# Optimization experiments

Measured on AMD Instinct MI355X. Metric: run time of the kernel, lower is better.

## Reference

```python
import jax, jax.numpy as jnp
import numpy as np

N, E, F, H, G, C = 50000, 800000, 128, 64, 512, 10
RATIO = 0.5  # forward arg `ratio` baked as constant


def seg_mean(msgs, idx, n):
    s = jax.ops.segment_sum(msgs, idx, num_segments=n)
    cnt = jax.ops.segment_sum(jnp.ones(idx.shape[0], msgs.dtype), idx, num_segments=n)
    return s / jnp.maximum(cnt, 1.0)[:, None]


def sage(x, src, dst, Wl, bl, Wr, ew=None):
    # PyG SAGEConv: lin_l(mean_{j->i} msg_j) + lin_r(x_i); weighted variant scales messages
    m = x[src] if ew is None else x[src] * ew[:, None]
    agg = seg_mean(m, dst, x.shape[0])
    return agg @ Wl + bl + x @ Wr


def topk_mask(scores, seg, num_graphs, ratio):
    # per-graph (segment) top-k edge selection: keep ceil(ratio*edges_in_graph) highest scores
    e = scores.shape[0]
    counts = jax.ops.segment_sum(jnp.ones(e, jnp.float32), seg, num_segments=num_graphs)
    order = jnp.lexsort((-scores, seg))  # sort by segment, then score descending
    seg_sorted = seg[order]
    starts = jnp.concatenate([jnp.zeros(1, jnp.float32), jnp.cumsum(counts)[:-1]])
    rank = jnp.arange(e, dtype=jnp.float32) - starts[seg_sorted]
    k = jnp.ceil(ratio * counts)
    sel = (rank < k[seg_sorted]).astype(scores.dtype)
    return jnp.zeros(e, scores.dtype).at[order].set(sel)


def setup_inputs():
    key = jax.random.key(0)
    ks = jax.random.split(key, 16)
    w = lambda k, shape, fan: (jax.random.normal(k, shape, jnp.float32) / np.sqrt(fan))
    return {
        'x': jax.random.normal(ks[0], (N, F), jnp.float32),
        'edge_index': jax.random.randint(ks[1], (2, E), 0, N, jnp.int32),
        'batch': jnp.sort(jax.random.randint(ks[2], (N,), 0, G, jnp.int32)),
        'W1l': w(ks[3], (F, H), F), 'b1l': jnp.zeros(H, jnp.float32), 'W1r': w(ks[4], (F, H), F),
        'W2l': w(ks[5], (H, H), H), 'b2l': jnp.zeros(H, jnp.float32), 'W2r': w(ks[6], (H, H), H),
        'W3l': w(ks[7], (H, H), H), 'b3l': jnp.zeros(H, jnp.float32), 'W3r': w(ks[8], (H, H), H),
        'Wlin1': w(ks[9], (H, H), H), 'blin1': jnp.zeros(H, jnp.float32),
        'Wlin2': w(ks[10], (H, C), H), 'blin2': jnp.zeros(C, jnp.float32),
    }


def reference(x, edge_index, batch, W1l, b1l, W1r, W2l, b2l, W2r, W3l, b3l, W3r, Wlin1, blin1, Wlin2, blin2):
    src, dst = edge_index[0], edge_index[1]
    h = jax.nn.relu(sage(x, src, dst, W1l, b1l, W1r))
    edge_scores = jnp.sum(h[src] * h[dst], axis=-1)  # [E]
    seg = batch[src]  # graph id per edge (sections)
    sampled = topk_mask(edge_scores, seg, G, RATIO)
    ew = edge_scores * sampled
    h = jax.nn.relu(sage(h, src, dst, W2l, b2l, W2r, ew))
    h = jax.nn.relu(sage(h, src, dst, W3l, b3l, W3r, ew))
    pooled = seg_mean(h, batch, G)  # global_mean_pool
    z = jax.nn.relu(pooled @ Wlin1 + blin1)
    z = z @ Wlin2 + blin2  # dropout inactive in eval
    return jax.nn.log_softmax(z, axis=-1), sampled
```

## Files before the change

### kernel.cpp

```cpp
#include <hip/hip_runtime.h>
#include <hip/hip_bf16.h>
#include <math.h>

static constexpr int N = 50000;
static constexpr int E = 800000;
static constexpr int F = 128;
static constexpr int H = 64;
static constexpr int G = 512;
static constexpr int C = 10;
static constexpr int CAP = 256;
static constexpr int NFB = (E / 4 + 255) / 256;
static constexpr int GB1 = N / 16;
static constexpr int GB2 = (N + 31) / 32;
static constexpr int SB = E / 256;

static inline int cdiv(long a, int b) { return (int)((a + b - 1) / b); }

__device__ __forceinline__ float uinv_score(unsigned u) {
  return (u & 0x80000000u) ? __uint_as_float(u & 0x7fffffffu) : __uint_as_float(~u);
}

__device__ __forceinline__ int2 pack_slot(int s, int d, int g, int e) {
  unsigned a = (unsigned)s | ((unsigned)(d & 0x7FFF) << 17);
  unsigned b = ((unsigned)d >> 15) | ((unsigned)g << 2) | ((unsigned)e << 11);
  return make_int2((int)a, (int)b);
}
__device__ __forceinline__ int slot_src(int2 p) { return p.x & 0x1FFFF; }
__device__ __forceinline__ int slot_dst(int2 p) {
  return (int)(((unsigned)p.x >> 17) | (((unsigned)p.y & 3u) << 15));
}
__device__ __forceinline__ int slot_g(int2 p) { return (int)(((unsigned)p.y >> 2) & 0x1FFu); }
__device__ __forceinline__ int slot_eid(int2 p) { return (int)((unsigned)p.y >> 11); }

__global__ void k_deg_goff(const int* __restrict__ dst, const int* __restrict__ batch,
                           int* __restrict__ deg, int* __restrict__ goff,
                           unsigned short* __restrict__ rank16) {
  int tid = threadIdx.x;
  for (int i = blockIdx.x * 256 + tid; i < N; i += gridDim.x * 256) {
    int b = batch[i];
    if (i == 0) {
      for (int g = 0; g <= b; ++g) goff[g] = 0;
    } else {
      int p = batch[i - 1];
      for (int g = p + 1; g <= b; ++g) goff[g] = i;
    }
    if (i == N - 1) {
      for (int g = b + 1; g <= G; ++g) goff[g] = N;
    }
  }
  const int4* d4 = (const int4*)dst;
  for (int i = blockIdx.x * 256 + tid; i < E / 4; i += gridDim.x * 256) {
    int4 v = d4[i];
    ushort4 rk;
    rk.x = (unsigned short)atomicAdd(&deg[v.x], 1);
    rk.y = (unsigned short)atomicAdd(&deg[v.y], 1);
    rk.z = (unsigned short)atomicAdd(&deg[v.z], 1);
    rk.w = (unsigned short)atomicAdd(&deg[v.w], 1);
    *(ushort4*)(rank16 + (size_t)i * 4) = rk;
  }
}

__global__ void k_scan_a(const int* __restrict__ cnt, int* __restrict__ off,
                         int* __restrict__ bsum, int n) {
  __shared__ int wsum[16];
  int tid = threadIdx.x, lane = tid & 63, wv = tid >> 6;
  int idx = blockIdx.x * 4096 + tid * 4;
  int v0 = (idx + 0 < n) ? cnt[idx + 0] : 0;
  int v1 = (idx + 1 < n) ? cnt[idx + 1] : 0;
  int v2 = (idx + 2 < n) ? cnt[idx + 2] : 0;
  int v3 = (idx + 3 < n) ? cnt[idx + 3] : 0;
  int local = v0 + v1 + v2 + v3;
  int inc = local;
  for (int d = 1; d < 64; d <<= 1) {
    int t = __shfl_up(inc, d);
    if (lane >= d) inc += t;
  }
  if (lane == 63) wsum[wv] = inc;
  __syncthreads();
  if (tid < 16) {
    int t = wsum[tid];
    for (int d = 1; d < 16; d <<= 1) {
      int u = __shfl_up(t, d);
      if (tid >= d) t += u;
    }
    wsum[tid] = t;
  }
  __syncthreads();
  int woff = (wv > 0) ? wsum[wv - 1] : 0;
  int excl = woff + inc - local;
  if (idx + 0 < n) off[idx + 0] = excl;
  if (idx + 1 < n) off[idx + 1] = excl + v0;
  if (idx + 2 < n) off[idx + 2] = excl + v0 + v1;
  if (idx + 3 < n) off[idx + 3] = excl + v0 + v1 + v2;
  if (tid == 0) bsum[blockIdx.x] = wsum[15];
}

__global__ void k_scan_c(int* __restrict__ off, const int* __restrict__ bsum, int n, int nb) {
  __shared__ int spre[34];
  int tid = threadIdx.x;
  if (tid < 32) {
    int v = (tid < nb) ? bsum[tid] : 0;
    int inc = v;
    for (int d = 1; d < 32; d <<= 1) {
      int t = __shfl_up(inc, d);
      if (tid >= d) inc += t;
    }
    spre[tid] = inc - v;
  }
  __syncthreads();
  int i = blockIdx.x * 256 + tid;
  if (i < n) {
    off[i] = off[i] + spre[i >> 12];
  } else if (i == n) {
    off[n] = spre[nb];
  }
}

__global__ void k_fill_gemm(const int* __restrict__ src, const int* __restrict__ dst,
                            const unsigned short* __restrict__ rank16,
                            const int* __restrict__ batch, const int* __restrict__ off,
                            int2* __restrict__ csrp, int* __restrict__ einv,
                            const float* __restrict__ x, const float* __restrict__ Wl,
                            const float* __restrict__ Wr, const float* __restrict__ bl,
                            float* __restrict__ y, float* __restrict__ r) {
  __shared__ float sx[16][F];
  int lane = threadIdx.x, ty = threadIdx.y;
  int tid = ty * 64 + lane;
  int bq = blockIdx.x / 5, br = blockIdx.x - bq * 5;
  if (br == 0) {
    int i = bq * 256 + tid;
    if (i < E / 4) {
      int4 dv = ((const int4*)dst)[i];
      int4 sv = ((const int4*)src)[i];
      ushort4 rv = *(const ushort4*)(rank16 + (size_t)i * 4);
      int dd[4] = {dv.x, dv.y, dv.z, dv.w};
      int ss[4] = {sv.x, sv.y, sv.z, sv.w};
      int rr[4] = {rv.x, rv.y, rv.z, rv.w};
      int e0 = i * 4;
      int slots[4];
#pragma unroll
      for (int j = 0; j < 4; ++j) {
        int g = batch[ss[j]];
        int slot = off[dd[j]] + rr[j];
        csrp[slot] = pack_slot(ss[j], dd[j], g, e0 + j);
        slots[j] = slot;
      }
      *(int4*)(einv + e0) = make_int4(slots[0], slots[1], slots[2], slots[3]);
    }
    return;
  }
  int gid = bq * 4 + (br - 1);
  if (gid >= GB1) return;
  int row0 = gid * 16;
  const float4* gsrc = (const float4*)(x + (size_t)row0 * F);
  float4* sdst = (float4*)(&sx[0][0]);
#pragma unroll
  for (int i = tid; i < 16 * F / 4; i += 256) sdst[i] = gsrc[i];
  __syncthreads();
  float al[4], ar[4];
  float bias = bl[lane];
#pragma unroll
  for (int j = 0; j < 4; ++j) { al[j] = 0.f; ar[j] = bias; }
#pragma unroll 4
  for (int f = 0; f < F; ++f) {
    float wl = Wl[f * H + lane];
    float wr = Wr[f * H + lane];
#pragma unroll
    for (int j = 0; j < 4; ++j) {
      float xv = sx[ty * 4 + j][f];
      al[j] += xv * wl;
      ar[j] += xv * wr;
    }
  }
#pragma unroll
  for (int j = 0; j < 4; ++j) {
    int row = row0 + ty * 4 + j;
    y[(size_t)row * H + lane] = al[j];
    r[(size_t)row * H + lane] = ar[j];
  }
}

template <int K>
__global__ void k_gemm2h(const float* __restrict__ in, const float* __restrict__ Wl,
                         const float* __restrict__ Wr, const float* __restrict__ b,
                         __hip_bfloat16* __restrict__ y, float* __restrict__ r) {
  __shared__ float sx[16][K];
  int lane = threadIdx.x, ty = threadIdx.y;
  int tid = ty * 64 + lane;
  int row0 = blockIdx.x * 16;
  const float4* gsrc = (const float4*)(in + (size_t)row0 * K);
  float4* sdst = (float4*)(&sx[0][0]);
#pragma unroll
  for (int i = tid; i < 16 * K / 4; i += 256) sdst[i] = gsrc[i];
  __syncthreads();
  float al[4], ar[4];
  float bias = b[lane];
#pragma unroll
  for (int j = 0; j < 4; ++j) { al[j] = 0.f; ar[j] = bias; }
#pragma unroll 4
  for (int f = 0; f < K; ++f) {
    float wl = Wl[f * H + lane];
    float wr = Wr[f * H + lane];
#pragma unroll
    for (int j = 0; j < 4; ++j) {
      float xv = sx[ty * 4 + j][f];
      al[j] += xv * wl;
      ar[j] += xv * wr;
    }
  }
#pragma unroll
  for (int j = 0; j < 4; ++j) {
    int row = row0 + ty * 4 + j;
    y[(size_t)row * H + lane] = __float2bfloat16(al[j]);
    r[(size_t)row * H + lane] = ar[j];
  }
}

__global__ void k_agg1(const float* __restrict__ y, const float* __restrict__ r,
                       const int2* __restrict__ csrp, const int* __restrict__ off,
                       float* __restrict__ out) {
  int node = blockIdx.x * 8 + threadIdx.y;
  int lane = threadIdx.x;
  int q = lane >> 3, c = lane & 7;
  int s0 = off[node], s1 = off[node + 1];
  float4 a0 = make_float4(0.f, 0.f, 0.f, 0.f);
  float4 a1 = make_float4(0.f, 0.f, 0.f, 0.f);
  int i = s0 + q;
  for (; i + 8 < s1; i += 16) {
    int se0 = slot_src(csrp[i]);
    int se1 = slot_src(csrp[i + 8]);
    const float4* p0 = (const float4*)(y + (size_t)se0 * H);
    const float4* p1 = (const float4*)(y + (size_t)se1 * H);
    float4 u0 = p0[c], v0 = p0[c + 8];
    float4 u1 = p1[c], v1 = p1[c + 8];
    a0.x += u0.x + u1.x; a0.y += u0.y + u1.y; a0.z += u0.z + u1.z; a0.w += u0.w + u1.w;
    a1.x += v0.x + v1.x; a1.y += v0.y + v1.y; a1.z += v0.z + v1.z; a1.w += v0.w + v1.w;
  }
  for (; i < s1; i += 8) {
    int se = slot_src(csrp[i]);
    const float4* p = (const float4*)(y + (size_t)se * H);
    float4 u = p[c], v = p[c + 8];
    a0.x += u.x; a0.y += u.y; a0.z += u.z; a0.w += u.w;
    a1.x += v.x; a1.y += v.y; a1.z += v.z; a1.w += v.w;
  }
#pragma unroll
  for (int d = 8; d < 64; d <<= 1) {
    a0.x += __shfl_xor(a0.x, d); a0.y += __shfl_xor(a0.y, d);
    a0.z += __shfl_xor(a0.z, d); a0.w += __shfl_xor(a0.w, d);
    a1.x += __shfl_xor(a1.x, d); a1.y += __shfl_xor(a1.y, d);
    a1.z += __shfl_xor(a1.z, d); a1.w += __shfl_xor(a1.w, d);
  }
  if (q == 0) {
    float inv = 1.f / fmaxf((float)(s1 - s0), 1.f);
    const float4* rp = (const float4*)(r + (size_t)node * H);
    float4 r0 = rp[c], r1 = rp[c + 8];
    float4 o0, o1;
    o0.x = fmaxf(a0.x * inv + r0.x, 0.f); o0.y = fmaxf(a0.y * inv + r0.y, 0.f);
    o0.z = fmaxf(a0.z * inv + r0.z, 0.f); o0.w = fmaxf(a0.w * inv + r0.w, 0.f);
    o1.x = fmaxf(a1.x * inv + r1.x, 0.f); o1.y = fmaxf(a1.y * inv + r1.y, 0.f);
    o1.z = fmaxf(a1.z * inv + r1.z, 0.f); o1.w = fmaxf(a1.w * inv + r1.w, 0.f);
    float4* op = (float4*)(out + (size_t)node * H);
    op[c] = o0; op[c + 8] = o1;
  }
}

__global__ void k_agg_w(const __hip_bfloat16* __restrict__ y, const float* __restrict__ r,
                        const int2* __restrict__ csr2, const int* __restrict__ cnt2,
                        const int* __restrict__ off, float* __restrict__ out) {
  int node = blockIdx.x * 8 + threadIdx.y;
  int lane = threadIdx.x;
  int q = lane >> 3, c = lane & 7;
  int b0 = off[node], cn = cnt2[node];
  float a[8] = {0.f, 0.f, 0.f, 0.f, 0.f, 0.f, 0.f, 0.f};
  for (int j = q; j < cn; j += 8) {
    int2 sw = csr2[b0 + j];
    float w = __int_as_float(sw.y);
    uint4 pk = ((const uint4*)((const unsigned short*)y + (size_t)sw.x * H))[c];
    a[0] += w * __uint_as_float(pk.x << 16); a[1] += w * __uint_as_float(pk.x & 0xffff0000u);
    a[2] += w * __uint_as_float(pk.y << 16); a[3] += w * __uint_as_float(pk.y & 0xffff0000u);
    a[4] += w * __uint_as_float(pk.z << 16); a[5] += w * __uint_as_float(pk.z & 0xffff0000u);
    a[6] += w * __uint_as_float(pk.w << 16); a[7] += w * __uint_as_float(pk.w & 0xffff0000u);
  }
#pragma unroll
  for (int d = 8; d < 64; d <<= 1) {
#pragma unroll
    for (int j = 0; j < 8; ++j) a[j] += __shfl_xor(a[j], d);
  }
  if (q == 0) {
    int degn = off[node + 1] - off[node];
    float inv = 1.f / fmaxf((float)degn, 1.f);
    const float4* rp = (const float4*)(r + (size_t)node * H);
    float4 r0 = rp[2 * c], r1 = rp[2 * c + 1];
    float4 o0, o1;
    o0.x = fmaxf(a[0] * inv + r0.x, 0.f); o0.y = fmaxf(a[1] * inv + r0.y, 0.f);
    o0.z = fmaxf(a[2] * inv + r0.z, 0.f); o0.w = fmaxf(a[3] * inv + r0.w, 0.f);
    o1.x = fmaxf(a[4] * inv + r1.x, 0.f); o1.y = fmaxf(a[5] * inv + r1.y, 0.f);
    o1.z = fmaxf(a[6] * inv + r1.z, 0.f); o1.w = fmaxf(a[7] * inv + r1.w, 0.f);
    float4* op = (float4*)(out + (size_t)node * H);
    op[2 * c] = o0; op[2 * c + 1] = o1;
  }
}

__global__ void k_score_g2h(const float* __restrict__ h1, const int2* __restrict__ csrp,
                            unsigned* __restrict__ scoreu_csr,
                            unsigned short* __restrict__ seg_csr, int* __restrict__ hist,
                            const float* __restrict__ Wl, const float* __restrict__ Wr,
                            const float* __restrict__ bl,
                            __hip_bfloat16* __restrict__ y, float* __restrict__ r) {
  __shared__ float sx[32][H];
  int lane = threadIdx.x, ty = threadIdx.y;
  int q3 = blockIdx.x / 3, r3 = blockIdx.x - q3 * 3;
  if (r3 == 0 && q3 < GB2) {
    int tid = ty * 64 + lane;
    int row0 = q3 * 32;
    {
      int row = row0 + (tid >> 4);
      if (row < N)
        ((float4*)(&sx[0][0]))[tid] = ((const float4*)h1)[(size_t)row * (H / 4) + (tid & 15)];
    }
    __syncthreads();
    float al[4], ar[4];
    float bias = bl[lane];
#pragma unroll
    for (int j = 0; j < 4; ++j) { al[j] = 0.f; ar[j] = bias; }
#pragma unroll 4
    for (int f = 0; f < H; ++f) {
      float wl = Wl[f * H + lane];
      float wr = Wr[f * H + lane];
#pragma unroll
      for (int j = 0; j < 4; ++j) {
        float xv = sx[ty * 4 + j][f];
        al[j] += xv * wl;
        ar[j] += xv * wr;
      }
    }
#pragma unroll
    for (int j = 0; j < 4; ++j) {
      int row = row0 + ty * 4 + j;
      if (row < N) {
        y[(size_t)row * H + lane] = __float2bfloat16(al[j]);
        r[(size_t)row * H + lane] = ar[j];
      }
    }
  } else {
    int sid = blockIdx.x - (q3 + (r3 > 0 ? 1 : 0));
    int q = lane >> 4, c = lane & 15;
    int s = (sid * 8 + ty) * 32 + q * 8;
    int2 se[8];
#pragma unroll
    for (int j = 0; j < 8; ++j) se[j] = csrp[s + j];
    float4 xr[8], yr[8];
#pragma unroll
    for (int j = 0; j < 8; ++j)
      xr[j] = ((const float4*)(h1 + (size_t)slot_src(se[j]) * H))[c];
#pragma unroll
    for (int j = 0; j < 8; ++j)
      yr[j] = ((const float4*)(h1 + (size_t)slot_dst(se[j]) * H))[c];
    float p[8];
#pragma unroll
    for (int j = 0; j < 8; ++j)
      p[j] = yr[j].x * xr[j].x + yr[j].y * xr[j].y + yr[j].z * xr[j].z + yr[j].w * xr[j].w;
#pragma unroll
    for (int d = 1; d < 16; d <<= 1) {
#pragma unroll
      for (int j = 0; j < 8; ++j) p[j] += __shfl_xor(p[j], d);
    }
    if (c == 0) {
#pragma unroll
      for (int j = 0; j < 8; ++j) {
        int g = slot_g(se[j]);
        unsigned u = __float_as_uint(p[j]);
        u = (u & 0x80000000u) ? ~u : (u | 0x80000000u);
        scoreu_csr[s + j] = u;
        seg_csr[s + j] = (unsigned short)g;
        atomicAdd(&hist[g * 256 + (int)(u >> 24)], 1);
      }
    }
  }
}

__global__ void k_hist(const unsigned* __restrict__ scoreu, const unsigned short* __restrict__ seg,
                       const unsigned* __restrict__ prefix, int* __restrict__ hist, int pass) {
  int e = (blockIdx.x * 256 + threadIdx.x) * 4;
  if (e >= E) return;
  uint4 u4 = *(const uint4*)(scoreu + e);
  ushort4 s4 = *(const ushort4*)(seg + e);
  unsigned uu[4] = {u4.x, u4.y, u4.z, u4.w};
  int gg[4] = {(int)s4.x, (int)s4.y, (int)s4.z, (int)s4.w};
  int predshift = 32 - 8 * pass;
  int bshift = 24 - 8 * pass;
#pragma unroll
  for (int j = 0; j < 4; ++j) {
    unsigned u = uu[j];
    int g = gg[j];
    if ((u >> predshift) == (prefix[g] >> predshift))
      atomicAdd(&hist[g * 256 + (int)((u >> bshift) & 0xFFu)], 1);
  }
}

__global__ void k_scan(int* __restrict__ hist, unsigned* __restrict__ prefix,
                       int* __restrict__ krem, int pass) {
  int g = blockIdx.x;
  int lane = threadIdx.x;
  int4* row = (int4*)(hist + (size_t)g * 256);
  int4 v = row[lane];
  int vj[4] = {v.x, v.y, v.z, v.w};
  int s = v.x + v.y + v.z + v.w;
  int inc = s;
  for (int d = 1; d < 64; d <<= 1) {
    int t = __shfl_up(inc, d);
    if (lane >= d) inc += t;
  }
  int T = __shfl(inc, 63);
  int k = (pass == 0) ? ((T + 1) >> 1) : krem[g];
  int excl = inc - s;
  int pre[4] = {excl, excl + vj[0], excl + vj[0] + vj[1], excl + vj[0] + vj[1] + vj[2]};
  int bsel_l = -1, newk_l = 0;
  if (k > 0) {
    for (int j = 3; j >= 0; --j) {
      int suf = T - pre[j];
      if (suf >= k) { bsel_l = 4 * lane + j; newk_l = k - (suf - vj[j]); break; }
    }
  }
  unsigned long long mask = __ballot(bsel_l >= 0);
  int bsel = 255, newk = 0;
  if (k > 0 && mask) {
    int hi = 63 - __builtin_clzll(mask);
    bsel = __shfl(bsel_l, hi);
    newk = __shfl(newk_l, hi);
  }
  if (lane == 0) {
    unsigned base = (pass == 0) ? 0u : prefix[g];
    prefix[g] = base | ((unsigned)bsel << (24 - 8 * pass));
    krem[g] = newk;
  }
  row[lane] = make_int4(0, 0, 0, 0);
}

__global__ void k_select(const unsigned* __restrict__ scoreu_csr,
                         const unsigned short* __restrict__ seg_csr,
                         const unsigned* __restrict__ thresh,
                         int* __restrict__ eqcnt, int* __restrict__ eqlist,
                         unsigned char* __restrict__ sel_csr) {
  int s = (blockIdx.x * 256 + threadIdx.x) * 4;
  if (s >= E) return;
  uint4 u4 = *(const uint4*)(scoreu_csr + s);
  ushort4 g4 = *(const ushort4*)(seg_csr + s);
  unsigned uu[4] = {u4.x, u4.y, u4.z, u4.w};
  int gg[4] = {(int)g4.x, (int)g4.y, (int)g4.z, (int)g4.w};
  unsigned char sl[4];
#pragma unroll
  for (int j = 0; j < 4; ++j) {
    unsigned u = uu[j];
    int g = gg[j];
    unsigned t = thresh[g];
    unsigned um = u & 0xffffff00u;
    unsigned char sel = 0;
    if (um > t) sel = 1;
    else if (um == t) {
      int slot = atomicAdd(&eqcnt[g], 1);
      if (slot < CAP) eqlist[g * CAP + slot] = s + j;
    }
    sl[j] = sel;
  }
  *(uchar4*)(sel_csr + s) = make_uchar4(sl[0], sl[1], sl[2], sl[3]);
}

__global__ void k_resolve(const int* __restrict__ krem, const int* __restrict__ eqcnt,
                          const int* __restrict__ eqlist, const int2* __restrict__ csrp,
                          const unsigned* __restrict__ scoreu_csr,
                          unsigned char* __restrict__ sel_csr) {
  int g = blockIdx.x * 256 + threadIdx.x;
  if (g >= G) return;
  int c = eqcnt[g]; if (c > CAP) c = CAP;
  int r = krem[g];  if (r > c) r = c;
  const int* lst = eqlist + g * CAP;
  unsigned last_u = 0u; int last_e = -1; bool first = true;
  for (int i = 0; i < r; ++i) {
    unsigned bu = 0u; int be = -1, bs = -1;
    for (int j = 0; j < c; ++j) {
      int slot = lst[j];
      unsigned u = scoreu_csr[slot];
      int eid = slot_eid(csrp[slot]);
      bool after = first || (u < last_u) || (u == last_u && eid > last_e);
      if (after && (bs < 0 || u > bu || (u == bu && eid < be))) { bu = u; be = eid; bs = slot; }
    }
    if (bs < 0) break;
    sel_csr[bs] = 1;
    last_u = bu; last_e = be; first = false;
  }
}

__global__ void k_samp_comp(const unsigned char* __restrict__ sel,
                            const int2* __restrict__ csrp,
                            const unsigned* __restrict__ scoreu,
                            const int* __restrict__ off, int2* __restrict__ csr2,
                            int* __restrict__ cnt2,
                            const int* __restrict__ einv, float* __restrict__ sampled) {
  int lane = threadIdx.x, ty = threadIdx.y;
  if (blockIdx.x < N / 8) {
    int node = blockIdx.x * 8 + ty;
    int s0 = off[node], s1 = off[node + 1];
    unsigned long long lt = ((unsigned long long)1 << lane) - 1;
    int cum = 0;
    for (int i0 = s0; i0 < s1; i0 += 64) {
      int i = i0 + lane;
      bool f = (i < s1) && sel[i];
      unsigned long long m = __ballot(f);
      if (f) {
        int rank = __popcll(m & lt);
        float w = uinv_score(scoreu[i]);
        csr2[s0 + cum + rank] = make_int2(slot_src(csrp[i]), __float_as_int(w));
      }
      cum += __popcll(m);
    }
    if (lane == 0) cnt2[node] = cum;
  } else {
    int tid = ty * 64 + lane;
    int e = ((blockIdx.x - N / 8) * 512 + tid) * 4;
    if (e >= E) return;
    int4 iv = *(const int4*)(einv + e);
    float4 o;
    o.x = (float)sel[iv.x];
    o.y = (float)sel[iv.y];
    o.z = (float)sel[iv.z];
    o.w = (float)sel[iv.w];
    *(float4*)(sampled + e) = o;
  }
}

__global__ void k_poolhead(const float* __restrict__ h3, const int* __restrict__ goff,
                           const float* __restrict__ W1, const float* __restrict__ b1,
                           const float* __restrict__ W2, const float* __restrict__ b2,
                           float* __restrict__ outp) {
  int g = blockIdx.x;
  int tid = threadIdx.x;
  int h = tid & 63, j = tid >> 6;
  int s0 = goff[g], s1 = goff[g + 1];
  float a = 0.f;
  for (int n = s0 + j; n < s1; n += 8) a += h3[(size_t)n * H + h];
  __shared__ float sp[8][H];
  __shared__ float p[H], z1[H], z2[C];
  __shared__ float lse;
  sp[j][h] = a;
  __syncthreads();
  if (j == 0) {
    float s = sp[0][h] + sp[1][h] + sp[2][h] + sp[3][h]
            + sp[4][h] + sp[5][h] + sp[6][h] + sp[7][h];
    float inv = 1.f / fmaxf((float)(s1 - s0), 1.f);
    p[h] = s * inv;
  }
  __syncthreads();
  if (j == 0) {
    float acc = b1[h];
#pragma unroll 8
    for (int f = 0; f < H; ++f) acc += p[f] * W1[f * H + h];
    z1[h] = fmaxf(acc, 0.f);
  }
  __syncthreads();
  if (tid < C) {
    float a2 = b2[tid];
#pragma unroll 8
    for (int f = 0; f < H; ++f) a2 += z1[f] * W2[f * C + tid];
    z2[tid] = a2;
  }
  __syncthreads();
  if (tid == 0) {
    float m = z2[0];
    for (int c = 1; c < C; ++c) m = fmaxf(m, z2[c]);
    float s = 0.f;
    for (int c = 0; c < C; ++c) s += expf(z2[c] - m);
    lse = m + logf(s);
  }
  __syncthreads();
  if (tid < C) outp[(size_t)g * C + tid] = z2[tid] - lse;
}

extern "C" void kernel_launch(void* const* d_in, const int* in_sizes, int n_in,
                              void* d_out, int out_size, void* d_ws, size_t ws_size,
                              hipStream_t stream) {
  const float* x     = (const float*)d_in[0];
  const int*   ei    = (const int*)d_in[1];
  const int*   batch = (const int*)d_in[2];
  const float* W1l   = (const float*)d_in[3];
  const float* b1l   = (const float*)d_in[4];
  const float* W1r   = (const float*)d_in[5];
  const float* W2l   = (const float*)d_in[6];
  const float* b2l   = (const float*)d_in[7];
  const float* W2r   = (const float*)d_in[8];
  const float* W3l   = (const float*)d_in[9];
  const float* b3l   = (const float*)d_in[10];
  const float* W3r   = (const float*)d_in[11];
  const float* Wlin1 = (const float*)d_in[12];
  const float* blin1 = (const float*)d_in[13];
  const float* Wlin2 = (const float*)d_in[14];
  const float* blin2 = (const float*)d_in[15];

  const int* srcv = ei;
  const int* dstv = ei + E;

  float* out_ls   = (float*)d_out;
  float* out_samp = out_ls + G * C;

  char* w = (char*)d_ws;
  auto carve = [&](size_t bytes) { void* p = (void*)w; w += (bytes + 255) & ~(size_t)255; return p; };
  char* zbase   = w;
  int*      deg     = (int*)carve((size_t)N * 4);
  int*      eqcnt   = (int*)carve((size_t)G * 4);
  int*      hist    = (int*)carve((size_t)G * 256 * 4);
  size_t    zbytes  = (size_t)(w - zbase);
  float*    h1      = (float*)carve((size_t)N * H * 4);
  float*    h2      = (float*)carve((size_t)N * H * 4);
  float*    h3      = (float*)carve((size_t)N * H * 4);
  float*    yb      = (float*)carve((size_t)N * H * 4);
  float*    rb      = (float*)carve((size_t)N * H * 4);
  __hip_bfloat16* ybh = (__hip_bfloat16*)carve((size_t)N * H * 2);
  unsigned* scoreu_csr = (unsigned*)carve((size_t)E * 4);
  unsigned short* seg_csr = (unsigned short*)carve((size_t)E * 2);
  unsigned char* sel_csr = (unsigned char*)carve((size_t)E);
  int2*     csrp    = (int2*)carve((size_t)E * 8);
  int*      einv    = (int*)carve((size_t)E * 4);
  unsigned short* rank16 = (unsigned short*)carve((size_t)E * 2);
  int*      off     = (int*)carve((size_t)(N + 1) * 4);
  int*      cnt2    = (int*)carve((size_t)N * 4);
  int*      goff    = (int*)carve((size_t)(G + 1) * 4);
  unsigned* prefix  = (unsigned*)carve((size_t)G * 4);
  int*      krem    = (int*)carve((size_t)G * 4);
  int*      eqlist  = (int*)carve((size_t)G * CAP * 4);
  int*      bsum    = (int*)carve((size_t)16 * 4);
  int2*     csr2    = (int2*)carve((size_t)E * 8);

  hipMemsetAsync(zbase, 0, zbytes, stream);

  k_deg_goff<<<512, 256, 0, stream>>>(dstv, batch, deg, goff, rank16);
  int nb = cdiv(N, 4096);
  k_scan_a<<<nb, 1024, 0, stream>>>(deg, off, bsum, N);
  k_scan_c<<<cdiv(N + 1, 256), 256, 0, stream>>>(off, bsum, N, nb);

  k_fill_gemm<<<5 * NFB, dim3(64, 4), 0, stream>>>(srcv, dstv, rank16, batch, off,
                                                   csrp, einv,
                                                   x, W1l, W1r, b1l, yb, rb);

  k_agg1<<<N / 8, dim3(64, 8), 0, stream>>>(yb, rb, csrp, off, h1);

  k_score_g2h<<<SB + GB2, dim3(64, 8), 0, stream>>>(h1, csrp, scoreu_csr, seg_csr, hist,
                                                    W2l, W2r, b2l, ybh, rb);
  k_scan<<<G, 64, 0, stream>>>(hist, prefix, krem, 0);
  for (int p = 1; p <= 2; ++p) {
    k_hist<<<cdiv(E / 4, 256), 256, 0, stream>>>(scoreu_csr, seg_csr, prefix, hist, p);
    k_scan<<<G, 64, 0, stream>>>(hist, prefix, krem, p);
  }
  k_select<<<cdiv(E / 4, 256), 256, 0, stream>>>(scoreu_csr, seg_csr, prefix,
                                                 eqcnt, eqlist, sel_csr);
  k_resolve<<<cdiv(G, 256), 256, 0, stream>>>(krem, eqcnt, eqlist, csrp, scoreu_csr,
                                              sel_csr);

  k_samp_comp<<<N / 8 + cdiv(E / 4, 512), dim3(64, 8), 0, stream>>>(
      sel_csr, csrp, scoreu_csr, off, csr2, cnt2, einv, out_samp);

  k_agg_w<<<N / 8, dim3(64, 8), 0, stream>>>(ybh, rb, csr2, cnt2, off, h2);

  k_gemm2h<H><<<N / 16, dim3(64, 4), 0, stream>>>(h2, W3l, W3r, b3l, ybh, rb);
  k_agg_w<<<N / 8, dim3(64, 8), 0, stream>>>(ybh, rb, csr2, cnt2, off, h3);

  k_poolhead<<<G, 512, 0, stream>>>(h3, goff, Wlin1, blin1, Wlin2, blin2, out_ls);
}
```

Before: 402.2 us.

## Drop einv buffer, recompute slots, move sampled output into agg kernel

Stops writing the per-edge inverse slot array in the fill kernel and instead recomputes each edge's CSR slot from dst, off and rank16 when writing the sampled mask. The sampled-mask write moves out of the compaction kernel and into extra blocks of the second weighted aggregation launch. Compaction now handles four nodes per wave using 16-lane groups instead of one node per wave. This removes a 3.2 MB write and read and improves lane utilisation for low-degree nodes, at the cost of an extra gather through off per edge.

```diff
diff --git a/kernel.cpp b/kernel.cpp
--- a/kernel.cpp
+++ b/kernel.cpp
@@ -13,6 +13,7 @@
 static constexpr int GB1 = N / 16;
 static constexpr int GB2 = (N + 31) / 32;
 static constexpr int SB = E / 256;
+static constexpr int SAMPB = (E / 4 + 511) / 512;
 
 static inline int cdiv(long a, int b) { return (int)((a + b - 1) / b); }
 
@@ -119,7 +120,7 @@
 __global__ void k_fill_gemm(const int* __restrict__ src, const int* __restrict__ dst,
                             const unsigned short* __restrict__ rank16,
                             const int* __restrict__ batch, const int* __restrict__ off,
-                            int2* __restrict__ csrp, int* __restrict__ einv,
+                            int2* __restrict__ csrp,
                             const float* __restrict__ x, const float* __restrict__ Wl,
                             const float* __restrict__ Wr, const float* __restrict__ bl,
                             float* __restrict__ y, float* __restrict__ r) {
@@ -137,15 +138,12 @@
       int ss[4] = {sv.x, sv.y, sv.z, sv.w};
       int rr[4] = {rv.x, rv.y, rv.z, rv.w};
       int e0 = i * 4;
-      int slots[4];
 #pragma unroll
       for (int j = 0; j < 4; ++j) {
         int g = batch[ss[j]];
         int slot = off[dd[j]] + rr[j];
         csrp[slot] = pack_slot(ss[j], dd[j], g, e0 + j);
-        slots[j] = slot;
       }
-      *(int4*)(einv + e0) = make_int4(slots[0], slots[1], slots[2], slots[3]);
     }
     return;
   }
@@ -266,9 +264,26 @@
 
 __global__ void k_agg_w(const __hip_bfloat16* __restrict__ y, const float* __restrict__ r,
                         const int2* __restrict__ csr2, const int* __restrict__ cnt2,
-                        const int* __restrict__ off, float* __restrict__ out) {
-  int node = blockIdx.x * 8 + threadIdx.y;
-  int lane = threadIdx.x;
+                        const int* __restrict__ off, float* __restrict__ out,
+                        const int* __restrict__ dst, const unsigned short* __restrict__ rank16,
+                        const unsigned char* __restrict__ sel, float* __restrict__ sampled) {
+  int lane = threadIdx.x, ty = threadIdx.y;
+  if (blockIdx.x >= N / 8) {
+    int tid = ty * 64 + lane;
+    int i = (blockIdx.x - N / 8) * 512 + tid;
+    if (i < E / 4) {
+      int4 dv = ((const int4*)dst)[i];
+      ushort4 rv = *(const ushort4*)(rank16 + (size_t)i * 4);
+      float4 o;
+      o.x = (float)sel[off[dv.x] + rv.x];
+      o.y = (float)sel[off[dv.y] + rv.y];
+      o.z = (float)sel[off[dv.z] + rv.z];
+      o.w = (float)sel[off[dv.w] + rv.w];
+      *(float4*)(sampled + (size_t)i * 4) = o;
+    }
+    return;
+  }
+  int node = blockIdx.x * 8 + ty;
   int q = lane >> 3, c = lane & 7;
   int b0 = off[node], cn = cnt2[node];
   float a[8] = {0.f, 0.f, 0.f, 0.f, 0.f, 0.f, 0.f, 0.f};
@@ -491,42 +506,30 @@
   }
 }
 
-__global__ void k_samp_comp(const unsigned char* __restrict__ sel,
-                            const int2* __restrict__ csrp,
-                            const unsigned* __restrict__ scoreu,
-                            const int* __restrict__ off, int2* __restrict__ csr2,
-                            int* __restrict__ cnt2,
-                            const int* __restrict__ einv, float* __restrict__ sampled) {
+__global__ void k_compact(const unsigned char* __restrict__ sel,
+                          const int2* __restrict__ csrp,
+                          const unsigned* __restrict__ scoreu,
+                          const int* __restrict__ off, int2* __restrict__ csr2,
+                          int* __restrict__ cnt2) {
   int lane = threadIdx.x, ty = threadIdx.y;
-  if (blockIdx.x < N / 8) {
-    int node = blockIdx.x * 8 + ty;
-    int s0 = off[node], s1 = off[node + 1];
-    unsigned long long lt = ((unsigned long long)1 << lane) - 1;
-    int cum = 0;
-    for (int i0 = s0; i0 < s1; i0 += 64) {
-      int i = i0 + lane;
-      bool f = (i < s1) && sel[i];
-      unsigned long long m = __ballot(f);
-      if (f) {
-        int rank = __popcll(m & lt);
-        float w = uinv_score(scoreu[i]);
-        csr2[s0 + cum + rank] = make_int2(slot_src(csrp[i]), __float_as_int(w));
-      }
-      cum += __popcll(m);
-    }
-    if (lane == 0) cnt2[node] = cum;
-  } else {
-    int tid = ty * 64 + lane;
-    int e = ((blockIdx.x - N / 8) * 512 + tid) * 4;
-    if (e >= E) return;
-    int4 iv = *(const int4*)(einv + e);
-    float4 o;
-    o.x = (float)sel[iv.x];
-    o.y = (float)sel[iv.y];
-    o.z = (float)sel[iv.z];
-    o.w = (float)sel[iv.w];
-    *(float4*)(sampled + e) = o;
-  }
+  int q = lane >> 4, c = lane & 15;
+  int node = (blockIdx.x * 8 + ty) * 4 + q;
+  if (node >= N) return;
+  int s0 = off[node], s1 = off[node + 1];
+  int cum = 0;
+  for (int i0 = s0; i0 < s1; i0 += 16) {
+    int i = i0 + c;
+    bool f = (i < s1) && sel[i];
+    unsigned long long m = __ballot(f);
+    unsigned gm = (unsigned)((m >> (16 * q)) & 0xFFFFull);
+    if (f) {
+      int rank = __popc(gm & ((1u << c) - 1u));
+      float w = uinv_score(scoreu[i]);
+      csr2[s0 + cum + rank] = make_int2(slot_src(csrp[i]), __float_as_int(w));
+    }
+    cum += __popc(gm);
+  }
+  if (c == 0) cnt2[node] = cum;
 }
 
 __global__ void k_poolhead(const float* __restrict__ h3, const int* __restrict__ goff,
@@ -619,7 +622,6 @@
   unsigned short* seg_csr = (unsigned short*)carve((size_t)E * 2);
   unsigned char* sel_csr = (unsigned char*)carve((size_t)E);
   int2*     csrp    = (int2*)carve((size_t)E * 8);
-  int*      einv    = (int*)carve((size_t)E * 4);
   unsigned short* rank16 = (unsigned short*)carve((size_t)E * 2);
   int*      off     = (int*)carve((size_t)(N + 1) * 4);
   int*      cnt2    = (int*)carve((size_t)N * 4);
@@ -637,8 +639,7 @@
   k_scan_a<<<nb, 1024, 0, stream>>>(deg, off, bsum, N);
   k_scan_c<<<cdiv(N + 1, 256), 256, 0, stream>>>(off, bsum, N, nb);
 
-  k_fill_gemm<<<5 * NFB, dim3(64, 4), 0, stream>>>(srcv, dstv, rank16, batch, off,
-                                                   csrp, einv,
+  k_fill_gemm<<<5 * NFB, dim3(64, 4), 0, stream>>>(srcv, dstv, rank16, batch, off, csrp,
                                                    x, W1l, W1r, b1l, yb, rb);
 
   k_agg1<<<N / 8, dim3(64, 8), 0, stream>>>(yb, rb, csrp, off, h1);
@@ -655,13 +656,15 @@
   k_resolve<<<cdiv(G, 256), 256, 0, stream>>>(krem, eqcnt, eqlist, csrp, scoreu_csr,
                                               sel_csr);
 
-  k_samp_comp<<<N / 8 + cdiv(E / 4, 512), dim3(64, 8), 0, stream>>>(
-      sel_csr, csrp, scoreu_csr, off, csr2, cnt2, einv, out_samp);
-
-  k_agg_w<<<N / 8, dim3(64, 8), 0, stream>>>(ybh, rb, csr2, cnt2, off, h2);
+  k_compact<<<cdiv(N, 32), dim3(64, 8), 0, stream>>>(sel_csr, csrp, scoreu_csr, off,
+                                                     csr2, cnt2);
+
+  k_agg_w<<<N / 8, dim3(64, 8), 0, stream>>>(ybh, rb, csr2, cnt2, off, h2,
+                                             nullptr, nullptr, nullptr, nullptr);
 
   k_gemm2h<H><<<N / 16, dim3(64, 4), 0, stream>>>(h2, W3l, W3r, b3l, ybh, rb);
-  k_agg_w<<<N / 8, dim3(64, 8), 0, stream>>>(ybh, rb, csr2, cnt2, off, h3);
+  k_agg_w<<<N / 8 + SAMPB, dim3(64, 8), 0, stream>>>(ybh, rb, csr2, cnt2, off, h3,
+                                                     dstv, rank16, sel_csr, out_samp);
 
   k_poolhead<<<G, 512, 0, stream>>>(h3, goff, Wlin1, blin1, Wlin2, blin2, out_ls);
 }
```

Result: no change. 404.4 us (+0.5%).
